# Optimization experiments

Measured on AMD Instinct MI355X. Metric: run time of the kernel, lower is better.

## Reference

```python
import jax, jax.numpy as jnp
import numpy as np

B, S, H = 1, 2048, 1024
NH, NKV, HD = 16, 4, 64
I, E, K = 2816, 8, 2
WIN = 512
EPS = 1e-5


def setup_inputs() -> dict:
    key = jax.random.key(0)
    ks = jax.random.split(key, 8)
    sd = 0.02
    return {
        "hidden_states": jax.random.normal(ks[0], (B, S, H), jnp.float32),
        "positions": jnp.arange(S, dtype=jnp.int64),
        "w_qkv": jax.random.normal(ks[1], ((NH + 2 * NKV) * HD, H), jnp.float32) * sd,
        "w_o": jax.random.normal(ks[2], (H, NH * HD), jnp.float32) * sd,
        "router_w": jax.random.normal(ks[3], (E, H), jnp.float32) * sd,
        "ws": jax.random.normal(ks[4], (E, 2 * I, H), jnp.float32) * sd,
        "w2s": jax.random.normal(ks[5], (E, H, I), jnp.float32) * sd,
        "ln1_w": jnp.ones((H,), jnp.float32),
        "ln2_w": jnp.ones((H,), jnp.float32),
    }


def _rmsnorm(x, w):
    return x * jax.lax.rsqrt(jnp.mean(x * x, axis=-1, keepdims=True) + EPS) * w


def reference(hidden_states, positions, w_qkv, w_o, router_w, ws, w2s, ln1_w, ln2_w):
    # residual is None on entry -> residual = input, then input_layernorm
    residual = hidden_states
    x = _rmsnorm(hidden_states, ln1_w)

    # qkv projection (torch Linear: y = x @ W.T), GQA split
    qkv = jnp.einsum("bsh,oh->bso", x, w_qkv)
    q_size, kv_size = NH * HD, NKV * HD
    q = qkv[..., :q_size].reshape(B, S, NH, HD)
    k = qkv[..., q_size:q_size + kv_size].reshape(B, S, NKV, HD)
    v = qkv[..., q_size + kv_size:].reshape(B, S, NKV, HD)
    rep = NH // NKV
    k = jnp.repeat(k, rep, axis=2)  # [B,S,NH,HD]
    v = jnp.repeat(v, rep, axis=2)

    scale = HD ** -0.5
    scores = jnp.einsum("bqhd,bkhd->bhqk", q, k) * scale
    i = jnp.arange(S)[:, None]
    j = jnp.arange(S)[None, :]
    mask = (j <= i) & ((i - j) < WIN)  # causal sliding window
    scores = jnp.where(mask, scores, jnp.finfo(scores.dtype).min)
    attn = jax.nn.softmax(scores, axis=-1)
    o = jnp.einsum("bhqk,bkhd->bqhd", attn, v).reshape(B, S, NH * HD)
    attn_out = jnp.einsum("bso,ho->bsh", o, w_o)

    # pre_moe_layernorm with residual: x += residual; residual = x; x = norm(x)
    x2 = attn_out + residual
    residual2 = x2
    h = _rmsnorm(x2, ln2_w)

    # MoE: router softmax, top-k (renormalize=False), per-expert SwiGLU FFN
    t = h.reshape(-1, H)  # [T,H]
    logits = jnp.einsum("th,eh->te", t, router_w)
    probs = jax.nn.softmax(logits, axis=-1)
    vals, idx = jax.lax.top_k(probs, K)  # [T,K]
    w_dense = jnp.sum(vals[:, :, None] * jax.nn.one_hot(idx, E, dtype=t.dtype), axis=1)  # [T,E]

    out = jnp.zeros_like(t)
    for e in range(E):
        gu = jnp.einsum("th,ih->ti", t, ws[e])  # [T,2I]
        g, u = gu[:, :I], gu[:, I:]
        a = jax.nn.silu(g) * u
        y = jnp.einsum("ti,hi->th", a, w2s[e])
        out = out + w_dense[:, e:e + 1] * y

    return out.reshape(B, S, H), residual2
```

## Files before the change

### kernel.cpp

```cpp
#include <hip/hip_runtime.h>
#include <stdint.h>

typedef unsigned short u16;
typedef __attribute__((ext_vector_type(8))) short short8;
typedef __attribute__((ext_vector_type(4))) float f32x4;

constexpr int SEQ   = 2048;
constexpr int HID   = 1024;
constexpr int NHEAD = 16;
constexpr int QKVD  = 1536;
constexpr int FFI   = 2816;
constexpr int NEXP  = 8;
constexpr int WINSZ = 512;
#define EPSF 1e-5f

__device__ __forceinline__ u16 f2bf(float f) {
  union { unsigned int i; float f; } v; v.f = f;
  unsigned int i = v.i;
  return (u16)((i + 0x7fffu + ((i >> 16) & 1u)) >> 16);
}

__device__ __forceinline__ void gload_lds16(const void* g, void* l) {
  __builtin_amdgcn_global_load_lds((__attribute__((address_space(1))) void*)g,
                                   (__attribute__((address_space(3))) void*)l,
                                   16, 0, 0);
}

#define MFMA_BF16(a, b, c) __builtin_amdgcn_mfma_f32_16x16x32_bf16(a, b, c, 0, 0, 0)

constexpr int CN1 = QKVD * HID / 4;
constexpr int CN2 = HID * HID / 4;
constexpr int CN3 = NEXP * 2 * FFI * HID / 4;
constexpr int CN4 = NEXP * HID * FFI / 4;
constexpr int CN_SMALL = CN1 + CN2;
constexpr int CN_BIG   = CN3 + CN4;
constexpr int NCONV_BLK = CN_BIG / 1024;
constexpr int NATTN_BLK = (SEQ / 64) * NHEAD;

__global__ __launch_bounds__(256) void k_prep(
    const float* __restrict__ x, const float* __restrict__ w, u16* __restrict__ y,
    const float* __restrict__ wqkv, const float* __restrict__ wo,
    u16* __restrict__ dq, u16* __restrict__ dwo) {
  const int bid = blockIdx.x, tid = threadIdx.x;
  __shared__ float red[4];
  if (bid < SEQ) {
    const int wid = tid >> 6, lane = tid & 63;
    const float* xr = x + (size_t)bid * HID;
    float4 v = *(const float4*)&xr[tid * 4];
    float ss = v.x * v.x + v.y * v.y + v.z * v.z + v.w * v.w;
#pragma unroll
    for (int m = 1; m < 64; m <<= 1) ss += __shfl_xor(ss, m);
    if (lane == 0) red[wid] = ss;
    __syncthreads();
    ss = red[0] + red[1] + red[2] + red[3];
    float sc = rsqrtf(ss * (1.0f / HID) + EPSF);
    float4 wv = *(const float4*)&w[tid * 4];
    ushort4 o;
    o.x = f2bf(v.x * sc * wv.x);
    o.y = f2bf(v.y * sc * wv.y);
    o.z = f2bf(v.z * sc * wv.z);
    o.w = f2bf(v.w * sc * wv.w);
    *(ushort4*)&y[(size_t)bid * HID + tid * 4] = o;
    return;
  }
  int j = (bid - SEQ) * 1024 + tid;
#pragma unroll
  for (int t = 0; t < 4; ++t) {
    int i = j + t * 256;
    const float* s; u16* d;
    if (i < CN1) { s = wqkv; d = dq; } else { i -= CN1; s = wo; d = dwo; }
    float4 v = ((const float4*)s)[i];
    ushort4 o;
    o.x = f2bf(v.x); o.y = f2bf(v.y); o.z = f2bf(v.z); o.w = f2bf(v.w);
    ((ushort4*)d)[i] = o;
  }
}

__global__ __launch_bounds__(256, 2) void k_gemm_bt(
    const u16* __restrict__ A, const u16* __restrict__ B,
    void* __restrict__ Cout, int N, int K, int wf32) {
  __shared__ u16 As[2][128 * 64];
  __shared__ u16 Bs[2][64 * 64];
  const int tid = threadIdx.x, wid = tid >> 6, lane = tid & 63;
  const int quad = lane >> 4, l16 = lane & 15;
  const int wr = wid >> 1, wc = wid & 1;
  const int m0 = blockIdx.y * 128, n0 = blockIdx.x * 64;
  const int sr = lane >> 3, sc = (lane & 7) * 8;
  f32x4 acc[4][2] = {};
  const int KT = K >> 6;

#define GSTAGE(buf, k0)                                                          \
  {                                                                              \
    _Pragma("unroll") for (int it = 0; it < 4; ++it) {                           \
      int seg = wid * 4 + it;                                                    \
      int row = seg * 8 + sr;                                                    \
      gload_lds16(&A[(size_t)(m0 + row) * K + (k0) + sc], &As[buf][seg * 512]);  \
    }                                                                            \
    _Pragma("unroll") for (int it = 0; it < 2; ++it) {                           \
      int seg = wid * 2 + it;                                                    \
      int row = seg * 8 + sr;                                                    \
      gload_lds16(&B[(size_t)(n0 + row) * K + (k0) + sc], &Bs[buf][seg * 512]);  \
    }                                                                            \
  }

  GSTAGE(0, 0);
  __syncthreads();
  int cur = 0;
  for (int kt = 0; kt < KT; ++kt) {
    if (kt + 1 < KT) GSTAGE(cur ^ 1, (kt + 1) << 6);
#pragma unroll
    for (int ks = 0; ks < 2; ++ks) {
      short8 af[4], bf[2];
#pragma unroll
      for (int t = 0; t < 4; ++t)
        af[t] = *(const short8*)&As[cur][(64 * wr + 16 * t + l16) * 64 + ks * 32 + quad * 8];
#pragma unroll
      for (int t = 0; t < 2; ++t)
        bf[t] = *(const short8*)&Bs[cur][(32 * wc + 16 * t + l16) * 64 + ks * 32 + quad * 8];
#pragma unroll
      for (int mt = 0; mt < 4; ++mt)
#pragma unroll
        for (int nt = 0; nt < 2; ++nt)
          acc[mt][nt] = MFMA_BF16(af[mt], bf[nt], acc[mt][nt]);
    }
    __syncthreads();
    cur ^= 1;
  }
#undef GSTAGE
  if (wf32) {
    float* C = (float*)Cout;
#pragma unroll
    for (int mt = 0; mt < 4; ++mt)
#pragma unroll
      for (int r = 0; r < 4; ++r) {
        int row = m0 + 64 * wr + 16 * mt + quad * 4 + r;
#pragma unroll
        for (int nt = 0; nt < 2; ++nt) {
          int col = n0 + 32 * wc + 16 * nt + l16;
          C[(size_t)row * N + col] = acc[mt][nt][r];
        }
      }
  } else {
    u16* C = (u16*)Cout;
#pragma unroll
    for (int mt = 0; mt < 4; ++mt)
#pragma unroll
      for (int r = 0; r < 4; ++r) {
        int row = m0 + 64 * wr + 16 * mt + quad * 4 + r;
#pragma unroll
        for (int nt = 0; nt < 2; ++nt) {
          int col = n0 + 32 * wc + 16 * nt + l16;
          C[(size_t)row * N + col] = f2bf(acc[mt][nt][r]);
        }
      }
  }
}

__global__ __launch_bounds__(256, 2) void k_attn_conv(
    const u16* __restrict__ qkv, u16* __restrict__ o,
    const float* __restrict__ ws, const float* __restrict__ w2s,
    u16* __restrict__ dws, u16* __restrict__ dw2) {
  const int bid = blockIdx.x;
  const int tid = threadIdx.x;
  if (bid >= NATTN_BLK) {
    int j = (bid - NATTN_BLK) * 1024 + tid;
#pragma unroll
    for (int t = 0; t < 4; ++t) {
      int i = j + t * 256;
      const float* s; u16* d;
      if (i < CN3) { s = ws; d = dws; } else { i -= CN3; s = w2s; d = dw2; }
      float4 v = ((const float4*)s)[i];
      ushort4 u;
      u.x = f2bf(v.x); u.y = f2bf(v.y); u.z = f2bf(v.z); u.w = f2bf(v.w);
      ((ushort4*)d)[i] = u;
    }
    return;
  }
  const int qb = bid & 31;
  const int h  = bid >> 5;
  const int q0 = qb * 64;
  const int g = h >> 2;
  __shared__ u16 Qs[64 * 72], Ks[64 * 72], Vt[64 * 72], Ps[64 * 72];
  const int wid = tid >> 6, lane = tid & 63;
  const int quad = lane >> 4, l16 = lane & 15;

#pragma unroll
  for (int it = 0; it < 2; ++it) {
    int idx = it * 256 + tid;
    int row = idx >> 3, c8 = (idx & 7) * 8;
    *(short8*)&Qs[row * 72 + c8] =
        *(const short8*)&qkv[(size_t)(q0 + row) * QKVD + h * 64 + c8];
  }

  f32x4 oacc[4] = {};
  float mrun[4], lrun[4];
#pragma unroll
  for (int r = 0; r < 4; ++r) { mrun[r] = -1e30f; lrun[r] = 0.f; }

  const int ktlo = (q0 >= WINSZ) ? ((q0 - WINSZ + 1) >> 6) : 0;
  const int kthi = qb;
  for (int kt = ktlo; kt <= kthi; ++kt) {
#pragma unroll
    for (int it = 0; it < 2; ++it) {
      int idx = it * 256 + tid;
      int row = idx >> 3, c8 = (idx & 7) * 8;
      *(short8*)&Ks[row * 72 + c8] =
          *(const short8*)&qkv[(size_t)(kt * 64 + row) * QKVD + 1024 + g * 64 + c8];
    }
#pragma unroll
    for (int it = 0; it < 8; ++it) {
      int idx = it * 256 + tid;
      int key = idx >> 5;
      int d = (idx & 31) * 2;
      unsigned int u = *(const unsigned int*)&qkv[(size_t)(kt * 64 + key) * QKVD + 1280 + g * 64 + d];
      Vt[d * 72 + key] = (u16)(u & 0xffffu);
      Vt[(d + 1) * 72 + key] = (u16)(u >> 16);
    }
    __syncthreads();

    f32x4 sa[4] = {};
#pragma unroll
    for (int ks = 0; ks < 2; ++ks) {
      short8 af = *(const short8*)&Qs[(16 * wid + l16) * 72 + ks * 32 + quad * 8];
#pragma unroll
      for (int ct = 0; ct < 4; ++ct) {
        short8 bf = *(const short8*)&Ks[(16 * ct + l16) * 72 + ks * 32 + quad * 8];
        sa[ct] = MFMA_BF16(af, bf, sa[ct]);
      }
    }

    float pvv[4][4];
#pragma unroll
    for (int r = 0; r < 4; ++r) {
      int i = q0 + 16 * wid + quad * 4 + r;
      float mx = -1e30f;
#pragma unroll
      for (int ct = 0; ct < 4; ++ct) {
        int j = kt * 64 + 16 * ct + l16;
        float v = sa[ct][r] * 0.125f;
        bool ok = (j <= i) && (i - j < WINSZ);
        v = ok ? v : -1e30f;
        pvv[ct][r] = v;
        mx = fmaxf(mx, v);
      }
#pragma unroll
      for (int m = 1; m < 16; m <<= 1) mx = fmaxf(mx, __shfl_xor(mx, m));
      float mnew = fmaxf(mrun[r], mx);
      float alpha = __expf(mrun[r] - mnew);
      float s = 0.f;
#pragma unroll
      for (int ct = 0; ct < 4; ++ct) {
        float p = (pvv[ct][r] > -1e29f) ? __expf(pvv[ct][r] - mnew) : 0.f;
        pvv[ct][r] = p;
        s += p;
      }
#pragma unroll
      for (int m = 1; m < 16; m <<= 1) s += __shfl_xor(s, m);
      lrun[r] = lrun[r] * alpha + s;
      mrun[r] = mnew;
#pragma unroll
      for (int ct = 0; ct < 4; ++ct) oacc[ct][r] *= alpha;
    }
#pragma unroll
    for (int ct = 0; ct < 4; ++ct)
#pragma unroll
      for (int r = 0; r < 4; ++r)
        Ps[(16 * wid + quad * 4 + r) * 72 + 16 * ct + l16] = f2bf(pvv[ct][r]);
    __syncthreads();

#pragma unroll
    for (int ks = 0; ks < 2; ++ks) {
      short8 af = *(const short8*)&Ps[(16 * wid + l16) * 72 + ks * 32 + quad * 8];
#pragma unroll
      for (int ct = 0; ct < 4; ++ct) {
        short8 bf = *(const short8*)&Vt[(16 * ct + l16) * 72 + ks * 32 + quad * 8];
        oacc[ct] = MFMA_BF16(af, bf, oacc[ct]);
      }
    }
    __syncthreads();
  }

#pragma unroll
  for (int ct = 0; ct < 4; ++ct)
#pragma unroll
    for (int r = 0; r < 4; ++r) {
      int row = q0 + 16 * wid + quad * 4 + r;
      float v = oacc[ct][r] / lrun[r];
      o[(size_t)row * HID + h * 64 + 16 * ct + l16] = f2bf(v);
    }
}

__global__ __launch_bounds__(256) void k_rms2_router(
    const float* __restrict__ of, const float* __restrict__ hs,
    const float* __restrict__ ln2, const float* __restrict__ rw,
    float* __restrict__ out1, u16* __restrict__ T, int* __restrict__ counts,
    int* __restrict__ tok_idx, int* __restrict__ tok_slot,
    float* __restrict__ tok_pw) {
  const int tkn = blockIdx.x, tid = threadIdx.x, wid = tid >> 6, lane = tid & 63;
  const size_t base = (size_t)tkn * HID + tid * 4;
  float4 a = *(const float4*)&of[base];
  float4 h = *(const float4*)&hs[base];
  float4 v;
  v.x = a.x + h.x; v.y = a.y + h.y; v.z = a.z + h.z; v.w = a.w + h.w;
  *(float4*)&out1[base] = v;
  float ss = v.x * v.x + v.y * v.y + v.z * v.z + v.w * v.w;
#pragma unroll
  for (int m = 1; m < 64; m <<= 1) ss += __shfl_xor(ss, m);
  __shared__ float red[4];
  if (lane == 0) red[wid] = ss;
  __syncthreads();
  ss = red[0] + red[1] + red[2] + red[3];
  float sc = rsqrtf(ss * (1.0f / HID) + EPSF);
  float4 lw = *(const float4*)&ln2[tid * 4];
  float t0 = v.x * sc * lw.x;
  float t1 = v.y * sc * lw.y;
  float t2 = v.z * sc * lw.z;
  float t3 = v.w * sc * lw.w;
  ushort4 o;
  o.x = f2bf(t0); o.y = f2bf(t1); o.z = f2bf(t2); o.w = f2bf(t3);
  *(ushort4*)&T[(size_t)tkn * HID + tid * 4] = o;

  float p[8];
#pragma unroll
  for (int e = 0; e < 8; ++e) {
    float4 r = *(const float4*)&rw[e * HID + tid * 4];
    p[e] = t0 * r.x + t1 * r.y + t2 * r.z + t3 * r.w;
  }
#pragma unroll
  for (int e = 0; e < 8; ++e)
#pragma unroll
    for (int m = 1; m < 64; m <<= 1) p[e] += __shfl_xor(p[e], m);
  __shared__ float pr[4][8];
  if (lane == 0)
#pragma unroll
    for (int e = 0; e < 8; ++e) pr[wid][e] = p[e];
  __syncthreads();
  if (tid == 0) {
    float lg[8];
#pragma unroll
    for (int e = 0; e < 8; ++e) lg[e] = pr[0][e] + pr[1][e] + pr[2][e] + pr[3][e];
    float mx = lg[0];
#pragma unroll
    for (int e = 1; e < 8; ++e) mx = fmaxf(mx, lg[e]);
    float ex[8], se = 0.f;
#pragma unroll
    for (int e = 0; e < 8; ++e) { ex[e] = __expf(lg[e] - mx); se += ex[e]; }
    int b0 = 0;
#pragma unroll
    for (int e = 1; e < 8; ++e) if (lg[e] > lg[b0]) b0 = e;
    int b1 = (b0 == 0) ? 1 : 0;
#pragma unroll
    for (int e = 0; e < 8; ++e) if (e != b0 && lg[e] > lg[b1]) b1 = e;
    float inv = 1.0f / se;
    int s0 = atomicAdd(&counts[b0], 1);
    tok_idx[b0 * SEQ + s0] = tkn;
    tok_slot[2 * tkn] = b0 * SEQ + s0;
    tok_pw[2 * tkn] = ex[b0] * inv;
    int s1 = atomicAdd(&counts[b1], 1);
    tok_idx[b1 * SEQ + s1] = tkn;
    tok_slot[2 * tkn + 1] = b1 * SEQ + s1;
    tok_pw[2 * tkn + 1] = ex[b1] * inv;
  }
}

__global__ void k_offsets(const int* __restrict__ counts, int* __restrict__ offs) {
  if (threadIdx.x == 0 && blockIdx.x == 0) {
    int s = 0;
    for (int e = 0; e < NEXP; ++e) { offs[e] = s; s += counts[e]; }
    offs[NEXP] = s;
  }
}

__global__ __launch_bounds__(256, 2) void k_moe_gu(
    const u16* __restrict__ T, const u16* __restrict__ Wgu,
    const int* __restrict__ counts, const int* __restrict__ offs,
    const int* __restrict__ tok_idx, u16* __restrict__ Abuf) {
  const int e = blockIdx.z;
  const int cnt = counts[e];
  const int m0 = blockIdx.y * 128;
  if (m0 >= cnt) return;
  const int n0 = blockIdx.x * 64;
  const u16* We = Wgu + (size_t)e * 2 * FFI * HID;
  const int* ti = tok_idx + e * SEQ;
  const int aoff = offs[e];
  __shared__ u16 As[2][128 * 64], Bg[2][64 * 64], Bu[2][64 * 64];
  const int tid = threadIdx.x, wid = tid >> 6, lane = tid & 63;
  const int quad = lane >> 4, l16 = lane & 15;
  const int wr = wid >> 1, wc = wid & 1;
  const int sr = lane >> 3, sc = (lane & 7) * 8;
  int tokrow[4];
#pragma unroll
  for (int it = 0; it < 4; ++it) {
    int row = (wid * 4 + it) * 8 + sr;
    int ra = m0 + row;
    if (ra > cnt - 1) ra = cnt - 1;
    tokrow[it] = ti[ra];
  }
  f32x4 accg[4][2] = {}, accu[4][2] = {};

#define MSTAGE(buf, k0)                                                            \
  {                                                                                \
    _Pragma("unroll") for (int it = 0; it < 4; ++it) {                             \
      int seg = wid * 4 + it;                                                      \
      gload_lds16(&T[(size_t)tokrow[it] * HID + (k0) + sc], &As[buf][seg * 512]);  \
    }                                                                              \
    _Pragma("unroll") for (int it = 0; it < 2; ++it) {                             \
      int seg = wid * 2 + it;                                                      \
      int row = seg * 8 + sr;                                                      \
      gload_lds16(&We[(size_t)(n0 + row) * HID + (k0) + sc], &Bg[buf][seg * 512]); \
      gload_lds16(&We[(size_t)(FFI + n0 + row) * HID + (k0) + sc],                 \
                  &Bu[buf][seg * 512]);                                            \
    }                                                                              \
  }

  MSTAGE(0, 0);
  __syncthreads();
  int cur = 0;
  for (int kt = 0; kt < 16; ++kt) {
    if (kt + 1 < 16) MSTAGE(cur ^ 1, (kt + 1) << 6);
#pragma unroll
    for (int ks = 0; ks < 2; ++ks) {
      short8 af[4], bg[2], bu[2];
#pragma unroll
      for (int t = 0; t < 4; ++t)
        af[t] = *(const short8*)&As[cur][(64 * wr + 16 * t + l16) * 64 + ks * 32 + quad * 8];
#pragma unroll
      for (int t = 0; t < 2; ++t) {
        bg[t] = *(const short8*)&Bg[cur][(32 * wc + 16 * t + l16) * 64 + ks * 32 + quad * 8];
        bu[t] = *(const short8*)&Bu[cur][(32 * wc + 16 * t + l16) * 64 + ks * 32 + quad * 8];
      }
#pragma unroll
      for (int mt = 0; mt < 4; ++mt)
#pragma unroll
        for (int nt = 0; nt < 2; ++nt) {
          accg[mt][nt] = MFMA_BF16(af[mt], bg[nt], accg[mt][nt]);
          accu[mt][nt] = MFMA_BF16(af[mt], bu[nt], accu[mt][nt]);
        }
    }
    __syncthreads();
    cur ^= 1;
  }
#undef MSTAGE
#pragma unroll
  for (int mt = 0; mt < 4; ++mt)
#pragma unroll
    for (int r = 0; r < 4; ++r) {
      int rl = 64 * wr + 16 * mt + quad * 4 + r;
      int grow = m0 + rl;
      if (grow < cnt) {
        size_t rbase = (size_t)(aoff + grow) * FFI;
#pragma unroll
        for (int nt = 0; nt < 2; ++nt) {
          int col = n0 + 32 * wc + 16 * nt + l16;
          float gv = accg[mt][nt][r];
          float uv = accu[mt][nt][r];
          float a = gv / (1.0f + __expf(-gv)) * uv;
          Abuf[rbase + col] = f2bf(a);
        }
      }
    }
}

__global__ __launch_bounds__(256, 2) void k_moe_y(
    const u16* __restrict__ Abuf, const u16* __restrict__ W2,
    const int* __restrict__ counts, const int* __restrict__ offs,
    float* __restrict__ ybuf) {
  const int e = blockIdx.z >> 1;
  const int sk = blockIdx.z & 1;
  const int cnt = counts[e];
  const int m0 = blockIdx.y * 128;
  if (m0 >= cnt) return;
  const int n0 = blockIdx.x * 128;
  const int kbase = sk * 1408;
  const u16* We = W2 + (size_t)e * HID * FFI;
  const int aoff = offs[e];
  __shared__ u16 As[2][128 * 64], Bs[2][128 * 64];
  const int tid = threadIdx.x, wid = tid >> 6, lane = tid & 63;
  const int quad = lane >> 4, l16 = lane & 15;
  const int wr = wid >> 1, wc = wid & 1;
  const int sr = lane >> 3, sc = (lane & 7) * 8;
  int arow[4];
#pragma unroll
  for (int it = 0; it < 4; ++it) {
    int row = (wid * 4 + it) * 8 + sr;
    int ra = m0 + row;
    if (ra > cnt - 1) ra = cnt - 1;
    arow[it] = aoff + ra;
  }
  f32x4 acc[4][4] = {};

#define YSTAGE(buf, k0)                                                             \
  {                                                                                 \
    _Pragma("unroll") for (int it = 0; it < 4; ++it) {                              \
      int seg = wid * 4 + it;                                                       \
      int row = seg * 8 + sr;                                                       \
      gload_lds16(&Abuf[(size_t)arow[it] * FFI + (k0) + sc], &As[buf][seg * 512]);  \
      gload_lds16(&We[(size_t)(n0 + row) * FFI + (k0) + sc], &Bs[buf][seg * 512]);  \
    }                                                                               \
  }

  YSTAGE(0, kbase);
  __syncthreads();
  int cur = 0;
  for (int kt = 0; kt < 22; ++kt) {
    if (kt + 1 < 22) YSTAGE(cur ^ 1, kbase + ((kt + 1) << 6));
#pragma unroll
    for (int ks = 0; ks < 2; ++ks) {
      short8 af[4], bf[4];
#pragma unroll
      for (int t = 0; t < 4; ++t)
        af[t] = *(const short8*)&As[cur][(64 * wr + 16 * t + l16) * 64 + ks * 32 + quad * 8];
#pragma unroll
      for (int t = 0; t < 4; ++t)
        bf[t] = *(const short8*)&Bs[cur][(64 * wc + 16 * t + l16) * 64 + ks * 32 + quad * 8];
#pragma unroll
      for (int mt = 0; mt < 4; ++mt)
#pragma unroll
        for (int nt = 0; nt < 4; ++nt)
          acc[mt][nt] = MFMA_BF16(af[mt], bf[nt], acc[mt][nt]);
    }
    __syncthreads();
    cur ^= 1;
  }
#undef YSTAGE
  float* Y = ybuf + (size_t)sk * 2 * SEQ * HID;
#pragma unroll
  for (int mt = 0; mt < 4; ++mt)
#pragma unroll
    for (int r = 0; r < 4; ++r) {
      int rl = 64 * wr + 16 * mt + quad * 4 + r;
      int grow = m0 + rl;
      if (grow < cnt) {
        size_t obase = (size_t)(aoff + grow) * HID;
#pragma unroll
        for (int nt = 0; nt < 4; ++nt) {
          int col = n0 + 64 * wc + 16 * nt + l16;
          Y[obase + col] = acc[mt][nt][r];
        }
      }
    }
}

__global__ __launch_bounds__(256) void k_moe_out(
    const float* __restrict__ yb, const int* __restrict__ offs,
    const int* __restrict__ tok_slot, const float* __restrict__ tok_pw,
    float* __restrict__ out0) {
  const int t = blockIdx.x, tid = threadIdx.x;
  const int v0 = tok_slot[2 * t], v1 = tok_slot[2 * t + 1];
  const float w0 = tok_pw[2 * t], w1 = tok_pw[2 * t + 1];
  const size_t g0 = (size_t)(offs[v0 >> 11] + (v0 & (SEQ - 1))) * HID;
  const size_t g1 = (size_t)(offs[v1 >> 11] + (v1 & (SEQ - 1))) * HID;
  const size_t YP = (size_t)2 * SEQ * HID;
  const int c = tid * 4;
  float4 a0 = *(const float4*)&yb[g0 + c];
  float4 b0 = *(const float4*)&yb[YP + g0 + c];
  float4 a1 = *(const float4*)&yb[g1 + c];
  float4 b1 = *(const float4*)&yb[YP + g1 + c];
  float4 r;
  r.x = w0 * (a0.x + b0.x) + w1 * (a1.x + b1.x);
  r.y = w0 * (a0.y + b0.y) + w1 * (a1.y + b1.y);
  r.z = w0 * (a0.z + b0.z) + w1 * (a1.z + b1.z);
  r.w = w0 * (a0.w + b0.w) + w1 * (a1.w + b1.w);
  *(float4*)&out0[(size_t)t * HID + c] = r;
}

extern "C" void kernel_launch(void* const* d_in, const int* in_sizes, int n_in,
                              void* d_out, int out_size, void* d_ws, size_t ws_size,
                              hipStream_t stream) {
  const float* hs   = (const float*)d_in[0];
  const float* wqkv = (const float*)d_in[2];
  const float* wo   = (const float*)d_in[3];
  const float* rwt  = (const float*)d_in[4];
  const float* wsx  = (const float*)d_in[5];
  const float* w2s  = (const float*)d_in[6];
  const float* ln1  = (const float*)d_in[7];
  const float* ln2  = (const float*)d_in[8];
  float* out0 = (float*)d_out;
  float* out1 = out0 + (size_t)SEQ * HID;

  char* p = (char*)d_ws;
  u16* xn       = (u16*)p;   p += (size_t)SEQ * HID * 2;
  u16* qkv      = (u16*)p;   p += (size_t)SEQ * QKVD * 2;
  u16* ob       = (u16*)p;   p += (size_t)SEQ * HID * 2;
  float* of     = (float*)p; p += (size_t)SEQ * HID * 4;
  int* counts   = (int*)p;   p += 32;
  int* offs     = (int*)p;   p += 64;
  int* tok_idx  = (int*)p;   p += (size_t)NEXP * SEQ * 4;
  int* tok_slot = (int*)p;   p += (size_t)2 * SEQ * 4;
  float* tok_pw = (float*)p; p += (size_t)2 * SEQ * 4;
  u16* abuf     = (u16*)p;   p += (size_t)2 * SEQ * FFI * 2;
  float* ybuf   = (float*)p; p += (size_t)2 * 2 * SEQ * HID * 4;
  u16* wqkv_b   = (u16*)p;   p += (size_t)QKVD * HID * 2;
  u16* wo_b     = (u16*)p;   p += (size_t)HID * HID * 2;
  u16* ws_b     = (u16*)p;   p += (size_t)NEXP * 2 * FFI * HID * 2;
  u16* w2s_b    = (u16*)p;   p += (size_t)NEXP * HID * FFI * 2;

  u16* tb = xn;

  hipMemsetAsync(counts, 0, 32, stream);

  k_prep<<<SEQ + CN_SMALL / 1024, 256, 0, stream>>>(
      hs, ln1, xn, wqkv, wo, wqkv_b, wo_b);
  k_gemm_bt<<<dim3(QKVD / 64, SEQ / 128), 256, 0, stream>>>(
      xn, wqkv_b, qkv, QKVD, HID, 0);
  k_attn_conv<<<NATTN_BLK + NCONV_BLK, 256, 0, stream>>>(
      qkv, ob, wsx, w2s, ws_b, w2s_b);
  k_gemm_bt<<<dim3(HID / 64, SEQ / 128), 256, 0, stream>>>(
      ob, wo_b, of, HID, HID, 1);
  k_rms2_router<<<SEQ, 256, 0, stream>>>(of, hs, ln2, rwt, out1, tb,
                                         counts, tok_idx, tok_slot, tok_pw);
  k_offsets<<<1, 64, 0, stream>>>(counts, offs);
  k_moe_gu<<<dim3(FFI / 64, SEQ / 128, NEXP), 256, 0, stream>>>(
      tb, ws_b, counts, offs, tok_idx, abuf);
  k_moe_y<<<dim3(HID / 128, SEQ / 128, NEXP * 2), 256, 0, stream>>>(
      abuf, w2s_b, counts, offs, ybuf);
  k_moe_out<<<SEQ, 256, 0, stream>>>(ybuf, offs, tok_slot, tok_pw, out0);
}
```

Measured before the change: 692.1 us.

## Drop GEMM double buffering, split-K the output projection, enlarge MoE gate-up tiles

All GEMM kernels switch from double-buffered LDS staging to a single buffer with a sync after each load, which halves LDS use so more blocks can be resident. The output-projection GEMM is split along K into two partial fp32 results, and the router kernel adds them together with the residual. The gate/up MoE kernel moves to 512-thread blocks covering 256 token rows with launch bounds (512,4). In exchange, global-load latency is no longer hidden behind compute, and the tighter launch bounds may force register spills or exceed the per-CU LDS budget.

```diff
diff --git a/kernel.cpp b/kernel.cpp
--- a/kernel.cpp
+++ b/kernel.cpp
@@ -78,45 +78,41 @@
 
 __global__ __launch_bounds__(256, 2) void k_gemm_bt(
     const u16* __restrict__ A, const u16* __restrict__ B,
-    void* __restrict__ Cout, int N, int K, int wf32) {
-  __shared__ u16 As[2][128 * 64];
-  __shared__ u16 Bs[2][64 * 64];
+    void* __restrict__ Cout, int N, int K, int KT, int wf32) {
+  __shared__ u16 As[128 * 64];
+  __shared__ u16 Bs[64 * 64];
   const int tid = threadIdx.x, wid = tid >> 6, lane = tid & 63;
   const int quad = lane >> 4, l16 = lane & 15;
   const int wr = wid >> 1, wc = wid & 1;
   const int m0 = blockIdx.y * 128, n0 = blockIdx.x * 64;
+  const int M = gridDim.y * 128;
+  const int kbase = blockIdx.z * KT * 64;
   const int sr = lane >> 3, sc = (lane & 7) * 8;
   f32x4 acc[4][2] = {};
-  const int KT = K >> 6;
-
-#define GSTAGE(buf, k0)                                                          \
-  {                                                                              \
-    _Pragma("unroll") for (int it = 0; it < 4; ++it) {                           \
-      int seg = wid * 4 + it;                                                    \
-      int row = seg * 8 + sr;                                                    \
-      gload_lds16(&A[(size_t)(m0 + row) * K + (k0) + sc], &As[buf][seg * 512]);  \
-    }                                                                            \
-    _Pragma("unroll") for (int it = 0; it < 2; ++it) {                           \
-      int seg = wid * 2 + it;                                                    \
-      int row = seg * 8 + sr;                                                    \
-      gload_lds16(&B[(size_t)(n0 + row) * K + (k0) + sc], &Bs[buf][seg * 512]);  \
-    }                                                                            \
-  }
-
-  GSTAGE(0, 0);
-  __syncthreads();
-  int cur = 0;
   for (int kt = 0; kt < KT; ++kt) {
-    if (kt + 1 < KT) GSTAGE(cur ^ 1, (kt + 1) << 6);
+    const int k0 = kbase + (kt << 6);
+#pragma unroll
+    for (int it = 0; it < 4; ++it) {
+      int seg = wid * 4 + it;
+      int row = seg * 8 + sr;
+      gload_lds16(&A[(size_t)(m0 + row) * K + k0 + sc], &As[seg * 512]);
+    }
+#pragma unroll
+    for (int it = 0; it < 2; ++it) {
+      int seg = wid * 2 + it;
+      int row = seg * 8 + sr;
+      gload_lds16(&B[(size_t)(n0 + row) * K + k0 + sc], &Bs[seg * 512]);
+    }
+    __syncthreads();
 #pragma unroll
     for (int ks = 0; ks < 2; ++ks) {
       short8 af[4], bf[2];
 #pragma unroll
       for (int t = 0; t < 4; ++t)
-        af[t] = *(const short8*)&As[cur][(64 * wr + 16 * t + l16) * 64 + ks * 32 + quad * 8];
+        af[t] = *(const short8*)&As[(64 * wr + 16 * t + l16) * 64 + ks * 32 + quad * 8];
 #pragma unroll
       for (int t = 0; t < 2; ++t)
-        bf[t] = *(const short8*)&Bs[cur][(32 * wc + 16 * t + l16) * 64 + ks * 32 + quad * 8];
+        bf[t] = *(const short8*)&Bs[(32 * wc + 16 * t + l16) * 64 + ks * 32 + quad * 8];
 #pragma unroll
       for (int mt = 0; mt < 4; ++mt)
 #pragma unroll
@@ -124,11 +120,9 @@
           acc[mt][nt] = MFMA_BF16(af[mt], bf[nt], acc[mt][nt]);
     }
     __syncthreads();
-    cur ^= 1;
-  }
-#undef GSTAGE
+  }
   if (wf32) {
-    float* C = (float*)Cout;
+    float* C = (float*)Cout + (size_t)blockIdx.z * M * N;
 #pragma unroll
     for (int mt = 0; mt < 4; ++mt)
 #pragma unroll
@@ -291,17 +285,20 @@
 }
 
 __global__ __launch_bounds__(256) void k_rms2_router(
-    const float* __restrict__ of, const float* __restrict__ hs,
-    const float* __restrict__ ln2, const float* __restrict__ rw,
-    float* __restrict__ out1, u16* __restrict__ T, int* __restrict__ counts,
+    const float* __restrict__ o0, const float* __restrict__ o1,
+    const float* __restrict__ hs, const float* __restrict__ ln2,
+    const float* __restrict__ rw, float* __restrict__ out1,
+    u16* __restrict__ T, int* __restrict__ counts,
     int* __restrict__ tok_idx, int* __restrict__ tok_slot,
     float* __restrict__ tok_pw) {
   const int tkn = blockIdx.x, tid = threadIdx.x, wid = tid >> 6, lane = tid & 63;
   const size_t base = (size_t)tkn * HID + tid * 4;
-  float4 a = *(const float4*)&of[base];
+  float4 a = *(const float4*)&o0[base];
+  float4 b = *(const float4*)&o1[base];
   float4 h = *(const float4*)&hs[base];
   float4 v;
-  v.x = a.x + h.x; v.y = a.y + h.y; v.z = a.z + h.z; v.w = a.w + h.w;
+  v.x = a.x + b.x + h.x; v.y = a.y + b.y + h.y;
+  v.z = a.z + b.z + h.z; v.w = a.w + b.w + h.w;
   *(float4*)&out1[base] = v;
   float ss = v.x * v.x + v.y * v.y + v.z * v.z + v.w * v.w;
 #pragma unroll
@@ -371,19 +368,19 @@
   }
 }
 
-__global__ __launch_bounds__(256, 2) void k_moe_gu(
+__global__ __launch_bounds__(512, 4) void k_moe_gu(
     const u16* __restrict__ T, const u16* __restrict__ Wgu,
     const int* __restrict__ counts, const int* __restrict__ offs,
     const int* __restrict__ tok_idx, u16* __restrict__ Abuf) {
   const int e = blockIdx.z;
   const int cnt = counts[e];
-  const int m0 = blockIdx.y * 128;
+  const int m0 = blockIdx.y * 256;
   if (m0 >= cnt) return;
   const int n0 = blockIdx.x * 64;
   const u16* We = Wgu + (size_t)e * 2 * FFI * HID;
   const int* ti = tok_idx + e * SEQ;
   const int aoff = offs[e];
-  __shared__ u16 As[2][128 * 64], Bg[2][64 * 64], Bu[2][64 * 64];
+  __shared__ u16 As[256 * 64], Bg[64 * 64], Bu[64 * 64];
   const int tid = threadIdx.x, wid = tid >> 6, lane = tid & 63;
   const int quad = lane >> 4, l16 = lane & 15;
   const int wr = wid >> 1, wc = wid & 1;
@@ -397,37 +394,29 @@
     tokrow[it] = ti[ra];
   }
   f32x4 accg[4][2] = {}, accu[4][2] = {};
-
-#define MSTAGE(buf, k0)                                                            \
-  {                                                                                \
-    _Pragma("unroll") for (int it = 0; it < 4; ++it) {                             \
-      int seg = wid * 4 + it;                                                      \
-      gload_lds16(&T[(size_t)tokrow[it] * HID + (k0) + sc], &As[buf][seg * 512]);  \
-    }                                                                              \
-    _Pragma("unroll") for (int it = 0; it < 2; ++it) {                             \
-      int seg = wid * 2 + it;                                                      \
-      int row = seg * 8 + sr;                                                      \
-      gload_lds16(&We[(size_t)(n0 + row) * HID + (k0) + sc], &Bg[buf][seg * 512]); \
-      gload_lds16(&We[(size_t)(FFI + n0 + row) * HID + (k0) + sc],                 \
-                  &Bu[buf][seg * 512]);                                            \
-    }                                                                              \
-  }
-
-  MSTAGE(0, 0);
-  __syncthreads();
-  int cur = 0;
   for (int kt = 0; kt < 16; ++kt) {
-    if (kt + 1 < 16) MSTAGE(cur ^ 1, (kt + 1) << 6);
+    const int k0 = kt << 6;
+#pragma unroll
+    for (int it = 0; it < 4; ++it) {
+      int seg = wid * 4 + it;
+      gload_lds16(&T[(size_t)tokrow[it] * HID + k0 + sc], &As[seg * 512]);
+    }
+    {
+      int row = wid * 8 + sr;
+      gload_lds16(&We[(size_t)(n0 + row) * HID + k0 + sc], &Bg[wid * 512]);
+      gload_lds16(&We[(size_t)(FFI + n0 + row) * HID + k0 + sc], &Bu[wid * 512]);
+    }
+    __syncthreads();
 #pragma unroll
     for (int ks = 0; ks < 2; ++ks) {
       short8 af[4], bg[2], bu[2];
 #pragma unroll
       for (int t = 0; t < 4; ++t)
-        af[t] = *(const short8*)&As[cur][(64 * wr + 16 * t + l16) * 64 + ks * 32 + quad * 8];
+        af[t] = *(const short8*)&As[(64 * wr + 16 * t + l16) * 64 + ks * 32 + quad * 8];
 #pragma unroll
       for (int t = 0; t < 2; ++t) {
-        bg[t] = *(const short8*)&Bg[cur][(32 * wc + 16 * t + l16) * 64 + ks * 32 + quad * 8];
-        bu[t] = *(const short8*)&Bu[cur][(32 * wc + 16 * t + l16) * 64 + ks * 32 + quad * 8];
+        bg[t] = *(const short8*)&Bg[(32 * wc + 16 * t + l16) * 64 + ks * 32 + quad * 8];
+        bu[t] = *(const short8*)&Bu[(32 * wc + 16 * t + l16) * 64 + ks * 32 + quad * 8];
       }
 #pragma unroll
       for (int mt = 0; mt < 4; ++mt)
@@ -438,9 +427,7 @@
         }
     }
     __syncthreads();
-    cur ^= 1;
-  }
-#undef MSTAGE
+  }
 #pragma unroll
   for (int mt = 0; mt < 4; ++mt)
 #pragma unroll
@@ -474,7 +461,7 @@
   const int kbase = sk * 1408;
   const u16* We = W2 + (size_t)e * HID * FFI;
   const int aoff = offs[e];
-  __shared__ u16 As[2][128 * 64], Bs[2][128 * 64];
+  __shared__ u16 As[128 * 64], Bs[128 * 64];
   const int tid = threadIdx.x, wid = tid >> 6, lane = tid & 63;
   const int quad = lane >> 4, l16 = lane & 15;
   const int wr = wid >> 1, wc = wid & 1;
@@ -488,31 +475,25 @@
     arow[it] = aoff + ra;
   }
   f32x4 acc[4][4] = {};
-
-#define YSTAGE(buf, k0)                                                             \
-  {                                                                                 \
-    _Pragma("unroll") for (int it = 0; it < 4; ++it) {                              \
-      int seg = wid * 4 + it;                                                       \
-      int row = seg * 8 + sr;                                                       \
-      gload_lds16(&Abuf[(size_t)arow[it] * FFI + (k0) + sc], &As[buf][seg * 512]);  \
-      gload_lds16(&We[(size_t)(n0 + row) * FFI + (k0) + sc], &Bs[buf][seg * 512]);  \
-    }                                                                               \
-  }
-
-  YSTAGE(0, kbase);
-  __syncthreads();
-  int cur = 0;
   for (int kt = 0; kt < 22; ++kt) {
-    if (kt + 1 < 22) YSTAGE(cur ^ 1, kbase + ((kt + 1) << 6));
+    const int k0 = kbase + (kt << 6);
+#pragma unroll
+    for (int it = 0; it < 4; ++it) {
+      int seg = wid * 4 + it;
+      int row = seg * 8 + sr;
+      gload_lds16(&Abuf[(size_t)arow[it] * FFI + k0 + sc], &As[seg * 512]);
+      gload_lds16(&We[(size_t)(n0 + row) * FFI + k0 + sc], &Bs[seg * 512]);
+    }
+    __syncthreads();
 #pragma unroll
     for (int ks = 0; ks < 2; ++ks) {
       short8 af[4], bf[4];
 #pragma unroll
       for (int t = 0; t < 4; ++t)
-        af[t] = *(const short8*)&As[cur][(64 * wr + 16 * t + l16) * 64 + ks * 32 + quad * 8];
+        af[t] = *(const short8*)&As[(64 * wr + 16 * t + l16) * 64 + ks * 32 + quad * 8];
 #pragma unroll
       for (int t = 0; t < 4; ++t)
-        bf[t] = *(const short8*)&Bs[cur][(64 * wc + 16 * t + l16) * 64 + ks * 32 + quad * 8];
+        bf[t] = *(const short8*)&Bs[(64 * wc + 16 * t + l16) * 64 + ks * 32 + quad * 8];
 #pragma unroll
       for (int mt = 0; mt < 4; ++mt)
 #pragma unroll
@@ -520,9 +501,7 @@
           acc[mt][nt] = MFMA_BF16(af[mt], bf[nt], acc[mt][nt]);
     }
     __syncthreads();
-    cur ^= 1;
-  }
-#undef YSTAGE
+  }
   float* Y = ybuf + (size_t)sk * 2 * SEQ * HID;
 #pragma unroll
   for (int mt = 0; mt < 4; ++mt)
@@ -582,7 +561,7 @@
   u16* xn       = (u16*)p;   p += (size_t)SEQ * HID * 2;
   u16* qkv      = (u16*)p;   p += (size_t)SEQ * QKVD * 2;
   u16* ob       = (u16*)p;   p += (size_t)SEQ * HID * 2;
-  float* of     = (float*)p; p += (size_t)SEQ * HID * 4;
+  float* of     = (float*)p; p += (size_t)2 * SEQ * HID * 4;
   int* counts   = (int*)p;   p += 32;
   int* offs     = (int*)p;   p += 64;
   int* tok_idx  = (int*)p;   p += (size_t)NEXP * SEQ * 4;
@@ -601,16 +580,17 @@
 
   k_prep<<<SEQ + CN_SMALL / 1024, 256, 0, stream>>>(
       hs, ln1, xn, wqkv, wo, wqkv_b, wo_b);
-  k_gemm_bt<<<dim3(QKVD / 64, SEQ / 128), 256, 0, stream>>>(
-      xn, wqkv_b, qkv, QKVD, HID, 0);
+  k_gemm_bt<<<dim3(QKVD / 64, SEQ / 128, 1), 256, 0, stream>>>(
+      xn, wqkv_b, qkv, QKVD, HID, 16, 0);
   k_attn_conv<<<NATTN_BLK + NCONV_BLK, 256, 0, stream>>>(
       qkv, ob, wsx, w2s, ws_b, w2s_b);
-  k_gemm_bt<<<dim3(HID / 64, SEQ / 128), 256, 0, stream>>>(
-      ob, wo_b, of, HID, HID, 1);
-  k_rms2_router<<<SEQ, 256, 0, stream>>>(of, hs, ln2, rwt, out1, tb,
-                                         counts, tok_idx, tok_slot, tok_pw);
+  k_gemm_bt<<<dim3(HID / 64, SEQ / 128, 2), 256, 0, stream>>>(
+      ob, wo_b, of, HID, HID, 8, 1);
+  k_rms2_router<<<SEQ, 256, 0, stream>>>(of, of + (size_t)SEQ * HID, hs, ln2,
+                                         rwt, out1, tb, counts, tok_idx,
+                                         tok_slot, tok_pw);
   k_offsets<<<1, 64, 0, stream>>>(counts, offs);
-  k_moe_gu<<<dim3(FFI / 64, SEQ / 128, NEXP), 256, 0, stream>>>(
+  k_moe_gu<<<dim3(FFI / 64, SEQ / 256, NEXP), 512, 0, stream>>>(
       tb, ws_b, counts, offs, tok_idx, abuf);
   k_moe_y<<<dim3(HID / 128, SEQ / 128, NEXP * 2), 256, 0, stream>>>(
       abuf, w2s_b, counts, offs, ybuf);
```

Result: no change. 678.6 us (-1.9%).
